# Kernel optimization log

Measured on AMD Instinct MI355X. Metric: run time of the kernel, lower is better.

Reference implementation:

```python
import jax, jax.numpy as jnp
import numpy as np
import math

B, IN, OUT = 32, 8192, 8192
DENSITY = 0.15

def _inverse_softplus(v):
    return math.log(math.expm1(v))

def setup_inputs() -> dict:
    key = jax.random.key(0)
    k1, k2, k3, k4 = jax.random.split(key, 4)
    inputs = jax.random.normal(k1, (B, IN), dtype=jnp.float32)
    active = jax.random.uniform(k2, (OUT, IN)) < DENSITY
    sign = jnp.where(jax.random.uniform(k3, (OUT, IN)) < 0.5, 1, -1)
    weight_state = jnp.where(active, sign, 0).astype(jnp.int32)
    # log_scale initialized so softplus(log_scale) = 1/sqrt(in_features)
    log_scale = jnp.full((OUT,), _inverse_softplus(1.0 / math.sqrt(IN)), dtype=jnp.float32)
    bias = jax.random.normal(k4, (OUT,), dtype=jnp.float32) * 0.01
    return {"inputs": inputs, "log_scale": log_scale, "bias": bias, "weight_state": weight_state}

def reference(inputs, log_scale, bias, weight_state):
    # scale = softplus(log_scale).clamp_min(1e-4), per output channel
    scale = jnp.maximum(jax.nn.softplus(log_scale), 1e-4)  # [OUT]
    # effective_weight = ternary_state * scale[:, None]; out = x @ W^T + b
    w = weight_state.astype(inputs.dtype) * scale[:, None]  # [OUT, IN]
    return jnp.einsum('bi,oi->bo', inputs, w) + bias
```

## Files before the change

kernel.cpp:

```cpp
#include <hip/hip_runtime.h>
#include <hip/hip_bf16.h>
#include <cmath>


#define K_SZ   8192
#define N_SZ   8192
#define B_SZ   32
#define KSPLIT 2
#define KHALF  (K_SZ / KSPLIT)
#define BN     32
#define BK     128
#define STEPS  (KHALF / BK)
#define LDW    132

typedef __attribute__((ext_vector_type(8))) short bf16x8;
typedef __attribute__((ext_vector_type(4))) float f32x4;

__device__ __forceinline__ unsigned pack_rn(float lo, float hi) {
  unsigned ul = __builtin_bit_cast(unsigned, lo) + 0x8000u;
  unsigned uh = __builtin_bit_cast(unsigned, hi) + 0x8000u;
  return (ul >> 16) | (uh & 0xFFFF0000u);
}
__device__ __forceinline__ unsigned pack_w(int w0, int w1) {
  unsigned u0 = __builtin_bit_cast(unsigned, (float)w0);
  unsigned u1 = __builtin_bit_cast(unsigned, (float)w1);
  return (u0 >> 16) | (u1 & 0xFFFF0000u);
}

__global__ void xprep(const float* __restrict__ X, uint4* __restrict__ Xr) {
  int t = blockIdx.x * blockDim.x + threadIdx.x;
  int lane = t & 63;
  int chunk = t >> 6;
  int kb = chunk >> 1;
  int mt = chunk & 1;
  int row = mt * 16 + (lane & 15);
  int k0 = kb * 32 + (lane >> 4) * 8;
  const float* p = X + (size_t)row * K_SZ + k0;
  float4 a = *(const float4*)p;
  float4 b = *(const float4*)(p + 4);
  uint4 o;
  o.x = pack_rn(a.x, a.y); o.y = pack_rn(a.z, a.w);
  o.z = pack_rn(b.x, b.y); o.w = pack_rn(b.z, b.w);
  Xr[t] = o;
}

__global__ __launch_bounds__(256, 2) void tmm(
    const int*   __restrict__ W,
    const uint4* __restrict__ Xr,
    const float* __restrict__ log_scale,
    const float* __restrict__ bias,
    float*       __restrict__ out) {
  __shared__ int lds[32 * LDW];

  const int tid  = threadIdx.x;
  const int w    = tid >> 6;
  const int lane = tid & 63;
  const int q    = lane >> 4;
  const int r    = lane & 15;
  const int nb   = blockIdx.x * BN;
  const int kh   = blockIdx.y;
  const int mt   = w & 1;
  const int nt   = w >> 1;

  const int srow = 8 * w + (lane >> 5);
  const int skof = 4 * (lane & 31);
  const int* gW = W + (size_t)(nb + srow) * K_SZ + (size_t)kh * KHALF + skof;
  const int lof = srow * LDW + skof;

  int4 wr0 = *(const int4*)(gW + 0 * 2 * K_SZ);
  int4 wr1 = *(const int4*)(gW + 1 * 2 * K_SZ);
  int4 wr2 = *(const int4*)(gW + 2 * 2 * K_SZ);
  int4 wr3 = *(const int4*)(gW + 3 * 2 * K_SZ);

  const uint4* xr = Xr + lane;
  const int kbb = kh * (KHALF / 32);
  uint4 a0 = xr[(size_t)((kbb + 0) * 2 + mt) * 64];
  uint4 a1 = xr[(size_t)((kbb + 1) * 2 + mt) * 64];
  uint4 a2 = xr[(size_t)((kbb + 2) * 2 + mt) * 64];
  uint4 a3 = xr[(size_t)((kbb + 3) * 2 + mt) * 64];

  f32x4 acc = {0.f, 0.f, 0.f, 0.f};
  const int Rbase = (nt * 16 + r) * LDW;

  for (int step = 0; step < STEPS; ++step) {
    __syncthreads();
    *(int4*)&lds[lof + 0 * 2 * LDW] = wr0;
    *(int4*)&lds[lof + 1 * 2 * LDW] = wr1;
    *(int4*)&lds[lof + 2 * 2 * LDW] = wr2;
    *(int4*)&lds[lof + 3 * 2 * LDW] = wr3;
    if (step + 1 < STEPS) {
      const int* g = gW + (step + 1) * BK;
      wr0 = *(const int4*)(g + 0 * 2 * K_SZ);
      wr1 = *(const int4*)(g + 1 * 2 * K_SZ);
      wr2 = *(const int4*)(g + 2 * 2 * K_SZ);
      wr3 = *(const int4*)(g + 3 * 2 * K_SZ);
    }
    __syncthreads();

    uint4 ca0 = a0, ca1 = a1, ca2 = a2, ca3 = a3;
    if (step + 1 < STEPS) {
      int kb2 = kbb + (step + 1) * 4;
      a0 = xr[(size_t)((kb2 + 0) * 2 + mt) * 64];
      a1 = xr[(size_t)((kb2 + 1) * 2 + mt) * 64];
      a2 = xr[(size_t)((kb2 + 2) * 2 + mt) * 64];
      a3 = xr[(size_t)((kb2 + 3) * 2 + mt) * 64];
    }

    #pragma unroll
    for (int s = 0; s < 4; ++s) {
      uint4 ca = (s == 0) ? ca0 : (s == 1) ? ca1 : (s == 2) ? ca2 : ca3;
      int ro = Rbase + s * 32 + q * 8;
      int4 b0 = *(const int4*)&lds[ro];
      int4 b1 = *(const int4*)&lds[ro + 4];
      union { unsigned u[4]; bf16x8 v; } Bf;
      Bf.u[0] = pack_w(b0.x, b0.y); Bf.u[1] = pack_w(b0.z, b0.w);
      Bf.u[2] = pack_w(b1.x, b1.y); Bf.u[3] = pack_w(b1.z, b1.w);
      bf16x8 Af = __builtin_bit_cast(bf16x8, ca);
      acc = __builtin_amdgcn_mfma_f32_16x16x32_bf16(Af, Bf.v, acc, 0, 0, 0);
    }
  }

  const int o = nb + nt * 16 + r;
  float sp    = log1pf(expf(log_scale[o]));
  float scale = fmaxf(sp, 1e-4f);
  float badd  = (kh == 0) ? bias[o] : 0.f;
  #pragma unroll
  for (int rg = 0; rg < 4; ++rg) {
    int b = mt * 16 + q * 4 + rg;
    atomicAdd(&out[(size_t)b * N_SZ + o], acc[rg] * scale + badd);
  }
}

extern "C" void kernel_launch(void* const* d_in, const int* in_sizes, int n_in,
                              void* d_out, int out_size, void* d_ws, size_t ws_size,
                              hipStream_t stream) {
  const float* X  = (const float*)d_in[0];
  const float* ls = (const float*)d_in[1];
  const float* bs = (const float*)d_in[2];
  const int*   W  = (const int*)d_in[3];
  float* out = (float*)d_out;
  uint4* Xr = (uint4*)d_ws;

  hipMemsetAsync(out, 0, (size_t)B_SZ * N_SZ * sizeof(float), stream);
  xprep<<<128, 256, 0, stream>>>(X, Xr);
  dim3 grid(N_SZ / BN, KSPLIT);
  tmm<<<grid, 256, 0, stream>>>(W, Xr, ls, bs, out);
}
```

Measured before the change: 366.3 us.

## Give each wave private bf16 LDS tile, widen N block and K split

Each wave now loads and owns 16 rows of the ternary weight tile and converts them to bf16 before storing into a private LDS slice. This removes the block-wide __syncthreads and halves LDS traffic. Each wave computes both 16-row batch tiles, so every B fragment feeds two MFMAs, and X fragments are loaded directly per step. The K split grows from 2 to 8 and the N block from 32 to 64, giving more blocks and more weight loads in flight to hide HBM latency on this bandwidth-bound kernel. The cost is four times as many atomicAdds into the output and higher register use per thread.

```diff
diff --git a/kernel.cpp b/kernel.cpp
--- a/kernel.cpp
+++ b/kernel.cpp
@@ -6,12 +6,12 @@
 #define K_SZ   8192
 #define N_SZ   8192
 #define B_SZ   32
-#define KSPLIT 2
-#define KHALF  (K_SZ / KSPLIT)
-#define BN     32
+#define KSPLIT 8
+#define KSPAN  (K_SZ / KSPLIT)
 #define BK     128
-#define STEPS  (KHALF / BK)
-#define LDW    132
+#define STEPS  (KSPAN / BK)
+#define BN     64
+#define LDB    136
 
 typedef __attribute__((ext_vector_type(8))) short bf16x8;
 typedef __attribute__((ext_vector_type(4))) float f32x4;
@@ -44,13 +44,13 @@
   Xr[t] = o;
 }
 
-__global__ __launch_bounds__(256, 2) void tmm(
+__global__ __launch_bounds__(256, 4) void tmm(
     const int*   __restrict__ W,
     const uint4* __restrict__ Xr,
     const float* __restrict__ log_scale,
     const float* __restrict__ bias,
     float*       __restrict__ out) {
-  __shared__ int lds[32 * LDW];
+  __shared__ unsigned short lds[4][16 * LDB];
 
   const int tid  = threadIdx.x;
   const int w    = tid >> 6;
@@ -59,75 +59,65 @@
   const int r    = lane & 15;
   const int nb   = blockIdx.x * BN;
   const int kh   = blockIdx.y;
-  const int mt   = w & 1;
-  const int nt   = w >> 1;
 
-  const int srow = 8 * w + (lane >> 5);
+  const int srow = lane >> 5;
   const int skof = 4 * (lane & 31);
-  const int* gW = W + (size_t)(nb + srow) * K_SZ + (size_t)kh * KHALF + skof;
-  const int lof = srow * LDW + skof;
+  const int* gW = W + (size_t)(nb + w * 16 + srow) * K_SZ + (size_t)kh * KSPAN + skof;
+  unsigned short* lw = &lds[w][0];
+  const int wofs = srow * LDB + skof;
 
-  int4 wr0 = *(const int4*)(gW + 0 * 2 * K_SZ);
-  int4 wr1 = *(const int4*)(gW + 1 * 2 * K_SZ);
-  int4 wr2 = *(const int4*)(gW + 2 * 2 * K_SZ);
-  int4 wr3 = *(const int4*)(gW + 3 * 2 * K_SZ);
+  int4 wr[8];
+  #pragma unroll
+  for (int j = 0; j < 8; ++j) wr[j] = *(const int4*)(gW + (size_t)j * 2 * K_SZ);
 
-  const uint4* xr = Xr + lane;
-  const int kbb = kh * (KHALF / 32);
-  uint4 a0 = xr[(size_t)((kbb + 0) * 2 + mt) * 64];
-  uint4 a1 = xr[(size_t)((kbb + 1) * 2 + mt) * 64];
-  uint4 a2 = xr[(size_t)((kbb + 2) * 2 + mt) * 64];
-  uint4 a3 = xr[(size_t)((kbb + 3) * 2 + mt) * 64];
-
-  f32x4 acc = {0.f, 0.f, 0.f, 0.f};
-  const int Rbase = (nt * 16 + r) * LDW;
+  f32x4 acc0 = {0.f,0.f,0.f,0.f};
+  f32x4 acc1 = {0.f,0.f,0.f,0.f};
+  const int rb = r * LDB;
+  const int kb_blk = kh * (KSPAN / 32);
 
   for (int step = 0; step < STEPS; ++step) {
-    __syncthreads();
-    *(int4*)&lds[lof + 0 * 2 * LDW] = wr0;
-    *(int4*)&lds[lof + 1 * 2 * LDW] = wr1;
-    *(int4*)&lds[lof + 2 * 2 * LDW] = wr2;
-    *(int4*)&lds[lof + 3 * 2 * LDW] = wr3;
+    uint2 p[8];
+    #pragma unroll
+    for (int j = 0; j < 8; ++j) {
+      p[j].x = pack_w(wr[j].x, wr[j].y);
+      p[j].y = pack_w(wr[j].z, wr[j].w);
+    }
     if (step + 1 < STEPS) {
       const int* g = gW + (step + 1) * BK;
-      wr0 = *(const int4*)(g + 0 * 2 * K_SZ);
-      wr1 = *(const int4*)(g + 1 * 2 * K_SZ);
-      wr2 = *(const int4*)(g + 2 * 2 * K_SZ);
-      wr3 = *(const int4*)(g + 3 * 2 * K_SZ);
+      #pragma unroll
+      for (int j = 0; j < 8; ++j) wr[j] = *(const int4*)(g + (size_t)j * 2 * K_SZ);
     }
-    __syncthreads();
+    #pragma unroll
+    for (int j = 0; j < 8; ++j)
+      *(uint2*)&lw[wofs + j * 2 * LDB] = p[j];
 
-    uint4 ca0 = a0, ca1 = a1, ca2 = a2, ca3 = a3;
-    if (step + 1 < STEPS) {
-      int kb2 = kbb + (step + 1) * 4;
-      a0 = xr[(size_t)((kb2 + 0) * 2 + mt) * 64];
-      a1 = xr[(size_t)((kb2 + 1) * 2 + mt) * 64];
-      a2 = xr[(size_t)((kb2 + 2) * 2 + mt) * 64];
-      a3 = xr[(size_t)((kb2 + 3) * 2 + mt) * 64];
+    const int kb0 = kb_blk + step * 4;
+    uint4 am[4][2];
+    #pragma unroll
+    for (int s = 0; s < 4; ++s) {
+      am[s][0] = Xr[(size_t)((kb0 + s) * 2 + 0) * 64 + lane];
+      am[s][1] = Xr[(size_t)((kb0 + s) * 2 + 1) * 64 + lane];
     }
 
     #pragma unroll
     for (int s = 0; s < 4; ++s) {
-      uint4 ca = (s == 0) ? ca0 : (s == 1) ? ca1 : (s == 2) ? ca2 : ca3;
-      int ro = Rbase + s * 32 + q * 8;
-      int4 b0 = *(const int4*)&lds[ro];
-      int4 b1 = *(const int4*)&lds[ro + 4];
-      union { unsigned u[4]; bf16x8 v; } Bf;
-      Bf.u[0] = pack_w(b0.x, b0.y); Bf.u[1] = pack_w(b0.z, b0.w);
-      Bf.u[2] = pack_w(b1.x, b1.y); Bf.u[3] = pack_w(b1.z, b1.w);
-      bf16x8 Af = __builtin_bit_cast(bf16x8, ca);
-      acc = __builtin_amdgcn_mfma_f32_16x16x32_bf16(Af, Bf.v, acc, 0, 0, 0);
+      bf16x8 Bf = *(const bf16x8*)&lw[rb + s * 32 + q * 8];
+      acc0 = __builtin_amdgcn_mfma_f32_16x16x32_bf16(
+                 __builtin_bit_cast(bf16x8, am[s][0]), Bf, acc0, 0, 0, 0);
+      acc1 = __builtin_amdgcn_mfma_f32_16x16x32_bf16(
+                 __builtin_bit_cast(bf16x8, am[s][1]), Bf, acc1, 0, 0, 0);
     }
   }
 
-  const int o = nb + nt * 16 + r;
+  const int o = nb + w * 16 + r;
   float sp    = log1pf(expf(log_scale[o]));
   float scale = fmaxf(sp, 1e-4f);
   float badd  = (kh == 0) ? bias[o] : 0.f;
   #pragma unroll
   for (int rg = 0; rg < 4; ++rg) {
-    int b = mt * 16 + q * 4 + rg;
-    atomicAdd(&out[(size_t)b * N_SZ + o], acc[rg] * scale + badd);
+    int b0 = q * 4 + rg;
+    atomicAdd(&out[(size_t)b0 * N_SZ + o],        acc0[rg] * scale + badd);
+    atomicAdd(&out[(size_t)(b0 + 16) * N_SZ + o], acc1[rg] * scale + badd);
   }
 }
 
```

After: 387.5 us. 5.8% more time.
